# Kernel tuning notes

Measured on AMD Instinct MI355X. Metric: run time of the kernel, lower is better.

## Reference

```python
import jax, jax.numpy as jnp
import numpy as np

D_MODEL = 1024
NUM_HEADS = 16
HEAD_DIM = D_MODEL // NUM_HEADS


def setup_inputs() -> dict:
    key = jax.random.key(0)
    ks = jax.random.split(key, 5)
    x = jax.random.normal(ks[0], (2, 2048, D_MODEL), dtype=jnp.float32)
    # torch.nn.Linear default init ~ U(-1/sqrt(fan_in), 1/sqrt(fan_in)); scale roughly
    s = 1.0 / np.sqrt(D_MODEL)
    W_qkv = jax.random.uniform(ks[1], (D_MODEL, 3 * D_MODEL), jnp.float32, -s, s)
    b_qkv = jax.random.uniform(ks[2], (3 * D_MODEL,), jnp.float32, -s, s)
    W_out = jax.random.uniform(ks[3], (D_MODEL, D_MODEL), jnp.float32, -s, s)
    b_out = jax.random.uniform(ks[4], (D_MODEL,), jnp.float32, -s, s)
    return {"x": x, "W_qkv": W_qkv, "b_qkv": b_qkv, "W_out": W_out, "b_out": b_out}


def reference(x, W_qkv, b_qkv, W_out, b_out):
    B, S, D = x.shape
    H, Hd = NUM_HEADS, HEAD_DIM
    qkv = x @ W_qkv + b_qkv                      # [B,S,3D]
    q, k, v = jnp.split(qkv, 3, axis=-1)
    def split_heads(t):
        return t.reshape(B, S, H, Hd).transpose(0, 2, 1, 3)  # [B,H,S,Hd]
    q, k, v = split_heads(q), split_heads(k), split_heads(v)
    scores = jnp.einsum('bhqd,bhkd->bhqk', q, k) / jnp.sqrt(jnp.float32(Hd))
    weights = jax.nn.softmax(scores, axis=-1)
    attn = jnp.einsum('bhqk,bhkd->bhqd', weights, v)
    attn = attn.transpose(0, 2, 1, 3).reshape(B, S, D)
    return attn @ W_out + b_out
```

## Files before the change

### kernel.cpp

```cpp
#include <hip/hip_runtime.h>
#include <hip/hip_bf16.h>

#define DMODEL 1024
#define NH 16
#define HD 64
#define SEQ 2048
#define BATCH 2
#define BH (BATCH * NH)
#define MTOT (BATCH * SEQ)

typedef _Float16 f16x8 __attribute__((ext_vector_type(8)));
typedef _Float16 f16x4 __attribute__((ext_vector_type(4)));
typedef _Float16 f16x2 __attribute__((ext_vector_type(2)));
typedef float f32x4 __attribute__((ext_vector_type(4)));
typedef float f32x16 __attribute__((ext_vector_type(16)));

__device__ __forceinline__ void gload_lds16(const void* g, void* l) {
  __builtin_amdgcn_global_load_lds((const __attribute__((address_space(1))) unsigned*)g,
                                   (__attribute__((address_space(3))) unsigned*)l, 16, 0, 0);
}

__global__ __launch_bounds__(256) void cvt_f2h(const float* __restrict__ in,
                                               _Float16* __restrict__ out, int n8) {
  const int i = blockIdx.x * 256 + threadIdx.x;
  if (i < n8) {
    const float4 a = ((const float4*)in)[i * 2];
    const float4 b = ((const float4*)in)[i * 2 + 1];
    f16x8 o = {(_Float16)a.x, (_Float16)a.y, (_Float16)a.z, (_Float16)a.w,
               (_Float16)b.x, (_Float16)b.y, (_Float16)b.z, (_Float16)b.w};
    *(f16x8*)&out[(size_t)i * 8] = o;
  }
}

__global__ __launch_bounds__(256) void cvt_transpose(const float* __restrict__ W,
                                                     _Float16* __restrict__ Wt,
                                                     int N, int K) {
  __shared__ float Ls[64][65];
  const int k0 = blockIdx.y * 64, n0 = blockIdx.x * 64;
  const int t = threadIdx.x;
  const int r = t >> 2, c4 = (t & 3) * 16;
#pragma unroll
  for (int j = 0; j < 4; ++j) {
    const float4 v = *(const float4*)&W[(size_t)(k0 + r) * N + n0 + c4 + j * 4];
    Ls[r][c4 + j * 4 + 0] = v.x;
    Ls[r][c4 + j * 4 + 1] = v.y;
    Ls[r][c4 + j * 4 + 2] = v.z;
    Ls[r][c4 + j * 4 + 3] = v.w;
  }
  __syncthreads();
  f16x8 o0, o1;
#pragma unroll
  for (int j = 0; j < 8; ++j) {
    o0[j] = (_Float16)Ls[c4 + j][r];
    o1[j] = (_Float16)Ls[c4 + 8 + j][r];
  }
  *(f16x8*)&Wt[(size_t)(n0 + r) * K + k0 + c4] = o0;
  *(f16x8*)&Wt[(size_t)(n0 + r) * K + k0 + c4 + 8] = o1;
}

__global__ __launch_bounds__(256) void qkv_mm(const _Float16* __restrict__ A,
                                              const _Float16* __restrict__ Bt,
                                              const float* __restrict__ bias,
                                              _Float16* __restrict__ qh,
                                              _Float16* __restrict__ kh,
                                              _Float16* __restrict__ vh) {
  __shared__ __align__(16) _Float16 As[128 * 64];
  __shared__ __align__(16) _Float16 Bs[128 * 64];
  const int t = threadIdx.x;
  const int w = t >> 6, lane = t & 63;
  const int g = lane >> 4, lr = lane & 15;
  const int m0 = blockIdx.y * 128, n0 = blockIdx.x * 128;
  const int wr = w >> 1, wc = w & 1;
  const int srow = (lane >> 3);
  const int col8 = (lane & 7) * 8;
  f32x4 acc[4][4] = {};

  for (int k0 = 0; k0 < DMODEL; k0 += 64) {
    __syncthreads();
#pragma unroll
    for (int i = 0; i < 4; ++i) {
      const int row = w * 32 + i * 8 + srow;
      gload_lds16(A + (size_t)(m0 + row) * DMODEL + k0 + col8, &As[(w * 4 + i) * 512]);
      gload_lds16(Bt + (size_t)(n0 + row) * DMODEL + k0 + col8, &Bs[(w * 4 + i) * 512]);
    }
    __syncthreads();
#pragma unroll
    for (int ks = 0; ks < 2; ++ks) {
      f16x8 af[4], bf[4];
#pragma unroll
      for (int mi = 0; mi < 4; ++mi)
        af[mi] = *(const f16x8*)&As[(wr * 64 + mi * 16 + lr) * 64 + ks * 32 + g * 8];
#pragma unroll
      for (int ni = 0; ni < 4; ++ni)
        bf[ni] = *(const f16x8*)&Bs[(wc * 64 + ni * 16 + lr) * 64 + ks * 32 + g * 8];
#pragma unroll
      for (int mi = 0; mi < 4; ++mi)
#pragma unroll
        for (int ni = 0; ni < 4; ++ni)
          acc[mi][ni] = __builtin_amdgcn_mfma_f32_16x16x32_f16(af[mi], bf[ni], acc[mi][ni], 0, 0, 0);
    }
  }

#pragma unroll
  for (int ni = 0; ni < 4; ++ni) {
    const int n = n0 + wc * 64 + ni * 16 + lr;
    const float bn = bias[n];
    const int which = n >> 10, d = n & 1023, h = d >> 6, hd = d & 63;
    _Float16* dst = which == 0 ? qh : which == 1 ? kh : vh;
    const float scale = which == 0 ? 0.18033688011f : 1.0f;
#pragma unroll
    for (int mi = 0; mi < 4; ++mi)
#pragma unroll
      for (int r = 0; r < 4; ++r) {
        const int m = m0 + wr * 64 + mi * 16 + g * 4 + r;
        const int bb = m >> 11, ss = m & 2047;
        dst[((size_t)(bb * NH + h) * SEQ + ss) * HD + hd] =
            (_Float16)((acc[mi][ni][r] + bn) * scale);
      }
  }
}

__device__ __forceinline__ void load_k(const _Float16* Kp, int kv0, int q, int hi,
                                       f16x8 (&kr)[8]) {
#pragma unroll
  for (int ks = 0; ks < 4; ++ks) {
    kr[2 * ks] = *(const f16x8*)(Kp + (size_t)(kv0 + q) * HD + ks * 16 + hi * 8);
    kr[2 * ks + 1] = *(const f16x8*)(Kp + (size_t)(kv0 + 32 + q) * HD + ks * 16 + hi * 8);
  }
}

__device__ __forceinline__ void load_v(const _Float16* Vp, int kv0, int skv, int sq4,
                                       f16x8 (&vr)[2]) {
  vr[0] = *(const f16x8*)(Vp + (size_t)(kv0 + skv) * HD + sq4 * 16);
  vr[1] = *(const f16x8*)(Vp + (size_t)(kv0 + skv) * HD + sq4 * 16 + 8);
}

__device__ __forceinline__ void store_v(_Float16 (*Vt)[76], int skv, int sq4,
                                        const f16x8 (&vr)[2]) {
#pragma unroll
  for (int e = 0; e < 8; ++e) {
    Vt[sq4 * 16 + e][skv] = vr[0][e];
    Vt[sq4 * 16 + 8 + e][skv] = vr[1][e];
  }
}

__device__ __forceinline__ void qkt(const f16x8 (&kr)[8], const f16x8 (&qf)[4],
                                    f32x16& s0, f32x16& s1) {
  s0 = {};
  s1 = {};
  __builtin_amdgcn_s_setprio(1);
#pragma unroll
  for (int ks = 0; ks < 4; ++ks) {
    s0 = __builtin_amdgcn_mfma_f32_32x32x16_f16(kr[2 * ks], qf[ks], s0, 0, 0, 0);
    s1 = __builtin_amdgcn_mfma_f32_32x32x16_f16(kr[2 * ks + 1], qf[ks], s1, 0, 0, 0);
  }
  __builtin_amdgcn_s_setprio(0);
}

__device__ __forceinline__ void softmax_update(f32x16& s0, f32x16& s1, float& mrun,
                                               float& lrun, f32x16& o0, f32x16& o1) {
  float tm[16];
#pragma unroll
  for (int r = 0; r < 16; ++r) tm[r] = fmaxf(s0[r], s1[r]);
#pragma unroll
  for (int d = 8; d > 0; d >>= 1)
#pragma unroll
    for (int r = 0; r < d; ++r) tm[r] = fmaxf(tm[r], tm[r + d]);
  const float mx = fmaxf(tm[0], __shfl_xor(tm[0], 32));
  if (!__all(mx <= mrun + 8.0f)) {
    const float mnew = fmaxf(mrun, mx);
    const float corr = exp2f(mrun - mnew);
    mrun = mnew;
    lrun *= corr;
#pragma unroll
    for (int r = 0; r < 16; ++r) {
      o0[r] *= corr;
      o1[r] *= corr;
    }
  }
#pragma unroll
  for (int r = 0; r < 16; ++r) {
    s0[r] = exp2f(s0[r] - mrun);
    s1[r] = exp2f(s1[r] - mrun);
  }
  float ts[16];
#pragma unroll
  for (int r = 0; r < 16; ++r) ts[r] = s0[r] + s1[r];
#pragma unroll
  for (int d = 8; d > 0; d >>= 1)
#pragma unroll
    for (int r = 0; r < d; ++r) ts[r] += ts[r + d];
  lrun += ts[0] + __shfl_xor(ts[0], 32);
}

__device__ __forceinline__ void pv(const f32x16& s0, const f32x16& s1,
                                   const _Float16 (*Vt)[76], int q, int hi,
                                   f32x16& o0, f32x16& o1) {
#pragma unroll
  for (int ks = 0; ks < 4; ++ks) {
    const int base = 8 * (ks & 1);
    unsigned u0, u1, u2, u3;
#pragma unroll
    for (int w01 = 0; w01 < 2; ++w01) {
      float a0, a1, b0, b1;
      if (ks < 2) {
        a0 = s0[base + 2 * w01];     a1 = s0[base + 2 * w01 + 1];
        b0 = s0[base + 4 + 2 * w01]; b1 = s0[base + 4 + 2 * w01 + 1];
      } else {
        a0 = s1[base + 2 * w01];     a1 = s1[base + 2 * w01 + 1];
        b0 = s1[base + 4 + 2 * w01]; b1 = s1[base + 4 + 2 * w01 + 1];
      }
      f16x2 hm0; hm0[0] = (_Float16)a0; hm0[1] = (_Float16)a1;
      f16x2 hm1; hm1[0] = (_Float16)b0; hm1[1] = (_Float16)b1;
      unsigned Pm0, Pm1;
      __builtin_memcpy(&Pm0, &hm0, 4);
      __builtin_memcpy(&Pm1, &hm1, 4);
      const unsigned local = hi ? Pm1 : Pm0;
      const unsigned sent = hi ? Pm0 : Pm1;
      const unsigned cross = __shfl_xor(sent, 32);
      const unsigned wa = hi ? cross : local;
      const unsigned wb = hi ? local : cross;
      if (w01 == 0) { u0 = wa; u2 = wb; } else { u1 = wa; u3 = wb; }
    }
    unsigned ww[4] = {u0, u1, u2, u3};
    f16x8 pb;
    __builtin_memcpy(&pb, ww, 16);
    const f16x8 va0 = *(const f16x8*)&Vt[0 + q][ks * 16 + hi * 8];
    const f16x8 va1 = *(const f16x8*)&Vt[32 + q][ks * 16 + hi * 8];
    __builtin_amdgcn_s_setprio(1);
    o0 = __builtin_amdgcn_mfma_f32_32x32x16_f16(va0, pb, o0, 0, 0, 0);
    o1 = __builtin_amdgcn_mfma_f32_32x32x16_f16(va1, pb, o1, 0, 0, 0);
    __builtin_amdgcn_s_setprio(0);
  }
}

__global__ __launch_bounds__(256, 2) void attn_fused(const _Float16* __restrict__ qh,
                                                     const _Float16* __restrict__ kh,
                                                     const _Float16* __restrict__ vh,
                                                     _Float16* __restrict__ ao) {
  __shared__ __align__(16) _Float16 Vt[2][64][76];
  const int t = threadIdx.x;
  const int lane = t & 63, w = t >> 6;
  const int q = lane & 31, hi = lane >> 5;
  const int bh = blockIdx.y;
  const int q0 = blockIdx.x * 128 + w * 32;
  const _Float16* Qp = qh + (size_t)bh * SEQ * HD;
  const _Float16* Kp = kh + (size_t)bh * SEQ * HD;
  const _Float16* Vp = vh + (size_t)bh * SEQ * HD;

  f16x8 qf[4];
#pragma unroll
  for (int ks = 0; ks < 4; ++ks)
    qf[ks] = *(const f16x8*)(Qp + (size_t)(q0 + q) * HD + ks * 16 + hi * 8);

  const int skv = t & 63;
  const int sq4 = t >> 6;

  f16x8 kA[8], kB[8], vA[2], vB[2];
  load_v(Vp, 0, skv, sq4, vA);
  load_k(Kp, 0, q, hi, kA);
  store_v(Vt[0], skv, sq4, vA);

  f32x16 o0 = {}, o1 = {};
  float mrun = -3e30f, lrun = 0.f;
  f32x16 s0, s1;

#pragma unroll 1
  for (int t2 = 0; t2 < 16; ++t2) {
    const int kvE = t2 * 128;
    qkt(kA, qf, s0, s1);
    load_v(Vp, kvE + 64, skv, sq4, vB);
    load_k(Kp, kvE + 64, q, hi, kB);
    softmax_update(s0, s1, mrun, lrun, o0, o1);
    __syncthreads();
    store_v(Vt[1], skv, sq4, vB);
    pv(s0, s1, Vt[0], q, hi, o0, o1);
    qkt(kB, qf, s0, s1);
    if (t2 < 15) {
      load_v(Vp, kvE + 128, skv, sq4, vA);
      load_k(Kp, kvE + 128, q, hi, kA);
    }
    softmax_update(s0, s1, mrun, lrun, o0, o1);
    __syncthreads();
    if (t2 < 15) store_v(Vt[0], skv, sq4, vA);
    pv(s0, s1, Vt[1], q, hi, o0, o1);
  }

  const float invl = 1.0f / lrun;
  _Float16* aob = ao + (size_t)bh * SEQ * HD + (size_t)(q0 + q) * HD;
#pragma unroll
  for (int m = 0; m < 4; ++m) {
    f16x4 v0, v1;
#pragma unroll
    for (int s2 = 0; s2 < 4; ++s2) {
      v0[s2] = (_Float16)(o0[4 * m + s2] * invl);
      v1[s2] = (_Float16)(o1[4 * m + s2] * invl);
    }
    *(f16x4*)(aob + 8 * m + 4 * hi) = v0;
    *(f16x4*)(aob + 32 + 8 * m + 4 * hi) = v1;
  }
}

__global__ __launch_bounds__(256) void out_mm(const _Float16* __restrict__ Ah,
                                              const _Float16* __restrict__ Bt,
                                              const float* __restrict__ bias,
                                              float* __restrict__ out) {
  __shared__ __align__(16) _Float16 As[128 * 64];
  __shared__ __align__(16) _Float16 Bs[128 * 64];
  const int t = threadIdx.x;
  const int w = t >> 6, lane = t & 63;
  const int g = lane >> 4, lr = lane & 15;
  const int m0 = blockIdx.y * 128, n0 = blockIdx.x * 128;
  const int wr = w >> 1, wc = w & 1;
  const int srow = (lane >> 3);
  const int col8 = (lane & 7) * 8;
  f32x4 acc[4][4] = {};

  for (int k0 = 0; k0 < DMODEL; k0 += 64) {
    const int h = k0 >> 6;
    __syncthreads();
#pragma unroll
    for (int i = 0; i < 4; ++i) {
      const int row = w * 32 + i * 8 + srow;
      const int m = m0 + row;
      const int bb = m >> 11, ss = m & 2047;
      gload_lds16(Ah + ((size_t)(bb * NH + h) * SEQ + ss) * HD + col8, &As[(w * 4 + i) * 512]);
      gload_lds16(Bt + (size_t)(n0 + row) * DMODEL + k0 + col8, &Bs[(w * 4 + i) * 512]);
    }
    __syncthreads();
#pragma unroll
    for (int ks = 0; ks < 2; ++ks) {
      f16x8 af[4], bf[4];
#pragma unroll
      for (int mi = 0; mi < 4; ++mi)
        af[mi] = *(const f16x8*)&As[(wr * 64 + mi * 16 + lr) * 64 + ks * 32 + g * 8];
#pragma unroll
      for (int ni = 0; ni < 4; ++ni)
        bf[ni] = *(const f16x8*)&Bs[(wc * 64 + ni * 16 + lr) * 64 + ks * 32 + g * 8];
#pragma unroll
      for (int mi = 0; mi < 4; ++mi)
#pragma unroll
        for (int ni = 0; ni < 4; ++ni)
          acc[mi][ni] = __builtin_amdgcn_mfma_f32_16x16x32_f16(af[mi], bf[ni], acc[mi][ni], 0, 0, 0);
    }
  }

#pragma unroll
  for (int ni = 0; ni < 4; ++ni) {
    const int n = n0 + wc * 64 + ni * 16 + lr;
    const float bn = bias[n];
#pragma unroll
    for (int mi = 0; mi < 4; ++mi)
#pragma unroll
      for (int r = 0; r < 4; ++r) {
        const int m = m0 + wr * 64 + mi * 16 + g * 4 + r;
        out[(size_t)m * DMODEL + n] = acc[mi][ni][r] + bn;
      }
  }
}

extern "C" void kernel_launch(void* const* d_in, const int* in_sizes, int n_in,
                              void* d_out, int out_size, void* d_ws, size_t ws_size,
                              hipStream_t stream) {
  const float* x = (const float*)d_in[0];
  const float* Wqkv = (const float*)d_in[1];
  const float* bqkv = (const float*)d_in[2];
  const float* Wout = (const float*)d_in[3];
  const float* bout = (const float*)d_in[4];
  float* out = (float*)d_out;

  char* ws = (char*)d_ws;
  const size_t MB = 1u << 20;
  _Float16* Xh = (_Float16*)(ws);
  _Float16* qh = (_Float16*)(ws + 8 * MB);
  _Float16* kh = (_Float16*)(ws + 16 * MB);
  _Float16* vh = (_Float16*)(ws + 24 * MB);
  _Float16* Wtq = (_Float16*)(ws + 32 * MB);
  _Float16* Wto = (_Float16*)(ws + 38 * MB + 512 * 1024);
  _Float16* attnh = Xh;

  cvt_f2h<<<dim3(MTOT * DMODEL / 8 / 256), 256, 0, stream>>>(x, Xh, MTOT * DMODEL / 8);
  cvt_transpose<<<dim3(3072 / 64, DMODEL / 64), 256, 0, stream>>>(Wqkv, Wtq, 3072, DMODEL);
  cvt_transpose<<<dim3(DMODEL / 64, DMODEL / 64), 256, 0, stream>>>(Wout, Wto, DMODEL, DMODEL);
  qkv_mm<<<dim3(3072 / 128, MTOT / 128), 256, 0, stream>>>(Xh, Wtq, bqkv, qh, kh, vh);
  attn_fused<<<dim3(SEQ / 128, BH), 256, 0, stream>>>(qh, kh, vh, attnh);
  out_mm<<<dim3(DMODEL / 128, MTOT / 128), 256, 0, stream>>>(attnh, Wto, bout, out);
}
```

Before: 268.5 us.

## Restructure attention pipeline with lighter barriers, XCD-aware block mapping, packed conversions

Reorders the attention main loop so the next K/V global loads are issued before LDS stores and compute. It replaces __syncthreads with a barrier that waits only on LDS counters, not on outstanding global loads, so prefetches can stay in flight across the barrier. The grid becomes 1D and is remapped so that consecutive blocks on the same XCD share batch-heads, aiming at better L2 reuse of K/V. The P matrix f16 packing now uses cvt_pkrtz, which rounds toward zero instead of to nearest. The last iteration issues a redundant wraparound prefetch in place of a branch.

```diff
diff --git a/kernel.cpp b/kernel.cpp
--- a/kernel.cpp
+++ b/kernel.cpp
@@ -11,13 +11,24 @@
 
 typedef _Float16 f16x8 __attribute__((ext_vector_type(8)));
 typedef _Float16 f16x4 __attribute__((ext_vector_type(4)));
-typedef _Float16 f16x2 __attribute__((ext_vector_type(2)));
+typedef __fp16 fp16x2 __attribute__((ext_vector_type(2)));
 typedef float f32x4 __attribute__((ext_vector_type(4)));
 typedef float f32x16 __attribute__((ext_vector_type(16)));
 
 __device__ __forceinline__ void gload_lds16(const void* g, void* l) {
   __builtin_amdgcn_global_load_lds((const __attribute__((address_space(1))) unsigned*)g,
                                    (__attribute__((address_space(3))) unsigned*)l, 16, 0, 0);
+}
+
+__device__ __forceinline__ void barrier_nodrain() {
+  asm volatile("s_waitcnt lgkmcnt(0)\n\ts_barrier" ::: "memory");
+}
+
+__device__ __forceinline__ unsigned pk16(float a, float b) {
+  const fp16x2 h = __builtin_amdgcn_cvt_pkrtz(a, b);
+  unsigned u;
+  __builtin_memcpy(&u, &h, 4);
+  return u;
 }
 
 __global__ __launch_bounds__(256) void cvt_f2h(const float* __restrict__ in,
@@ -210,11 +221,8 @@
         a0 = s1[base + 2 * w01];     a1 = s1[base + 2 * w01 + 1];
         b0 = s1[base + 4 + 2 * w01]; b1 = s1[base + 4 + 2 * w01 + 1];
       }
-      f16x2 hm0; hm0[0] = (_Float16)a0; hm0[1] = (_Float16)a1;
-      f16x2 hm1; hm1[0] = (_Float16)b0; hm1[1] = (_Float16)b1;
-      unsigned Pm0, Pm1;
-      __builtin_memcpy(&Pm0, &hm0, 4);
-      __builtin_memcpy(&Pm1, &hm1, 4);
+      const unsigned Pm0 = pk16(a0, a1);
+      const unsigned Pm1 = pk16(b0, b1);
       const unsigned local = hi ? Pm1 : Pm0;
       const unsigned sent = hi ? Pm0 : Pm1;
       const unsigned cross = __shfl_xor(sent, 32);
@@ -238,12 +246,15 @@
                                                      const _Float16* __restrict__ kh,
                                                      const _Float16* __restrict__ vh,
                                                      _Float16* __restrict__ ao) {
-  __shared__ __align__(16) _Float16 Vt[2][64][76];
+  __shared__ __align__(16) _Float16 Vt0[64][76];
+  __shared__ __align__(16) _Float16 Vt1[64][76];
   const int t = threadIdx.x;
   const int lane = t & 63, w = t >> 6;
   const int q = lane & 31, hi = lane >> 5;
-  const int bh = blockIdx.y;
-  const int q0 = blockIdx.x * 128 + w * 32;
+  const int wgid = blockIdx.x;
+  const int bh = (wgid & 7) * 4 + ((wgid >> 3) & 3);
+  const int qt = wgid >> 5;
+  const int q0 = qt * 128 + w * 32;
   const _Float16* Qp = qh + (size_t)bh * SEQ * HD;
   const _Float16* Kp = kh + (size_t)bh * SEQ * HD;
   const _Float16* Vp = vh + (size_t)bh * SEQ * HD;
@@ -253,37 +264,37 @@
   for (int ks = 0; ks < 4; ++ks)
     qf[ks] = *(const f16x8*)(Qp + (size_t)(q0 + q) * HD + ks * 16 + hi * 8);
 
+  f32x16 o0 = {}, o1 = {};
+  float mrun = -3e30f, lrun = 0.f;
+  f32x16 s0, s1;
+
   const int skv = t & 63;
   const int sq4 = t >> 6;
 
   f16x8 kA[8], kB[8], vA[2], vB[2];
   load_v(Vp, 0, skv, sq4, vA);
   load_k(Kp, 0, q, hi, kA);
-  store_v(Vt[0], skv, sq4, vA);
-
-  f32x16 o0 = {}, o1 = {};
-  float mrun = -3e30f, lrun = 0.f;
-  f32x16 s0, s1;
 
 #pragma unroll 1
   for (int t2 = 0; t2 < 16; ++t2) {
     const int kvE = t2 * 128;
-    qkt(kA, qf, s0, s1);
     load_v(Vp, kvE + 64, skv, sq4, vB);
     load_k(Kp, kvE + 64, q, hi, kB);
+    store_v(Vt0, skv, sq4, vA);
+    qkt(kA, qf, s0, s1);
     softmax_update(s0, s1, mrun, lrun, o0, o1);
-    __syncthreads();
-    store_v(Vt[1], skv, sq4, vB);
-    pv(s0, s1, Vt[0], q, hi, o0, o1);
+    barrier_nodrain();
+    pv(s0, s1, Vt0, q, hi, o0, o1);
+    {
+      const int nxt = (kvE + 128) & (SEQ - 1);
+      load_v(Vp, nxt, skv, sq4, vA);
+      load_k(Kp, nxt, q, hi, kA);
+    }
+    store_v(Vt1, skv, sq4, vB);
     qkt(kB, qf, s0, s1);
-    if (t2 < 15) {
-      load_v(Vp, kvE + 128, skv, sq4, vA);
-      load_k(Kp, kvE + 128, q, hi, kA);
-    }
     softmax_update(s0, s1, mrun, lrun, o0, o1);
-    __syncthreads();
-    if (t2 < 15) store_v(Vt[0], skv, sq4, vA);
-    pv(s0, s1, Vt[1], q, hi, o0, o1);
+    barrier_nodrain();
+    pv(s0, s1, Vt1, q, hi, o0, o1);
   }
 
   const float invl = 1.0f / lrun;
@@ -383,6 +394,6 @@
   cvt_transpose<<<dim3(3072 / 64, DMODEL / 64), 256, 0, stream>>>(Wqkv, Wtq, 3072, DMODEL);
   cvt_transpose<<<dim3(DMODEL / 64, DMODEL / 64), 256, 0, stream>>>(Wout, Wto, DMODEL, DMODEL);
   qkv_mm<<<dim3(3072 / 128, MTOT / 128), 256, 0, stream>>>(Xh, Wtq, bqkv, qh, kh, vh);
-  attn_fused<<<dim3(SEQ / 128, BH), 256, 0, stream>>>(qh, kh, vh, attnh);
+  attn_fused<<<dim3(512), 256, 0, stream>>>(qh, kh, vh, attnh);
   out_mm<<<dim3(DMODEL / 128, MTOT / 128), 256, 0, stream>>>(attnh, Wto, bout, out);
 }
```

New measurement: 263.8 us. About the same (-1.7%).
